# Kernel tuning notes

Measured on AMD Instinct MI355X. Metric: run time of the kernel, lower is better.

## Reference

```python
import jax, jax.numpy as jnp
import numpy as np

N, E, CIN, H, OUT, L, G = 100000, 1600000, 64, 128, 16, 3, 64

def setup_inputs() -> dict:
    key = jax.random.key(0)
    ks = jax.random.split(key, 20)
    def xav(k, shape):
        fan_in, fan_out = shape[-2], shape[-1]
        lim = float(np.sqrt(6.0 / (fan_in + fan_out)))
        return jax.random.uniform(k, shape, jnp.float32, -lim, lim)
    inp = {
        "x": jax.random.normal(ks[0], (N, CIN), jnp.float32),
        "pos": jax.random.normal(ks[1], (N, 3), jnp.float32),
        "edge_index": jax.random.randint(ks[2], (2, E), 0, N, jnp.int64),
        "batch": jnp.sort(jax.random.randint(ks[3], (N,), 0, G, jnp.int64)),
        # node_lin: Linear(CIN+3, H) -> ReLU -> Linear(H, H)
        "node_w1": xav(ks[4], (CIN + 3, H)), "node_b1": jnp.zeros((H,), jnp.float32),
        "node_w2": xav(ks[5], (H, H)), "node_b2": jnp.zeros((H,), jnp.float32),
        # L convs, each with [L, H, H] propagation weights and a GRUCell
        "conv_w": xav(ks[6], (L, L, H, H)),
        "gru_wih": xav(ks[7], (L, 3 * H, H)), "gru_whh": xav(ks[8], (L, 3 * H, H)),
        "gru_bih": jnp.zeros((L, 3 * H), jnp.float32), "gru_bhh": jnp.zeros((L, 3 * H), jnp.float32),
        "lin1_w": xav(ks[9], (H, H // 2)), "lin1_b": jnp.zeros((H // 2,), jnp.float32),
        "lin2_w": xav(ks[10], (H // 2, OUT)), "lin2_b": jnp.zeros((OUT,), jnp.float32),
    }
    return inp

def _gru_cell(m, h, wih, whh, bih, bhh):
    # torch.nn.GRUCell semantics: gates = [r, z, n]
    gi = m @ wih.T + bih  # [N, 3H]
    gh = h @ whh.T + bhh
    ir, iz, inn = jnp.split(gi, 3, axis=1)
    hr, hz, hn = jnp.split(gh, 3, axis=1)
    r = jax.nn.sigmoid(ir + hr)
    z = jax.nn.sigmoid(iz + hz)
    n = jnp.tanh(inn + r * hn)
    return (1.0 - z) * n + z * h

def reference(x, pos, edge_index, batch, node_w1, node_b1, node_w2, node_b2,
              conv_w, gru_wih, gru_whh, gru_bih, gru_bhh,
              lin1_w, lin1_b, lin2_w, lin2_b):
    src, dst = edge_index[0], edge_index[1]  # message flows src -> dst
    h = jnp.concatenate([x, pos], axis=1)
    h = jax.nn.relu(h @ node_w1 + node_b1) @ node_w2 + node_b2
    for l in range(L):  # GatedNet outer convs
        for i in range(L):  # GatedGraphConv inner iterations
            m = h @ conv_w[l, i]                                  # [N, H]
            agg = jax.ops.segment_sum(m[src], dst, num_segments=N)  # gather + scatter-add
            h = _gru_cell(agg, h, gru_wih[l], gru_whh[l], gru_bih[l], gru_bhh[l])
        h = jax.nn.relu(h)
    h = jax.nn.relu(h @ lin1_w + lin1_b)
    h = h @ lin2_w + lin2_b                                        # [N, OUT]
    return jax.ops.segment_sum(h, batch, num_segments=G)           # graph readout 'add'
```

## Files before the change

### kernel.cpp

```cpp
#include <hip/hip_runtime.h>

#define NN 100000
#define NE 1600000
#define NG 64
#define MAXDEG 64

typedef long long i64;
typedef unsigned short u16;
typedef unsigned int u32;
typedef __attribute__((ext_vector_type(8))) _Float16 f16x8;
typedef __attribute__((ext_vector_type(4))) _Float16 half4;
typedef __attribute__((ext_vector_type(4))) float f32x4;

__device__ __forceinline__ float sigm(float x){ return 1.f/(1.f+__expf(-x)); }
__device__ __forceinline__ float tanh_(float x){ return 2.f/(1.f+__expf(-2.f*x)) - 1.f; }
__device__ __forceinline__ f32x4 mfma16h(f16x8 a, f16x8 b, f32x4 c){
  return __builtin_amdgcn_mfma_f32_16x16x32_f16(a,b,c,0,0,0);
}
__device__ __forceinline__ u16 h2u(_Float16 h){ return *(const u16*)&h; }

__global__ __launch_bounds__(512) void k_detect(const int* __restrict__ ei,
    const int* __restrict__ batch, int* __restrict__ flags){
  int t = threadIdx.x;
  __shared__ int nz_e, nz_b;
  if (t == 0){ nz_e = 0; nz_b = 0; }
  __syncthreads();
  if (ei[2*t + 1] != 0) nz_e = 1;
  int k = NN/2 - 512 + t;
  if (batch[2*k + 1] != 0) nz_b = 1;
  __syncthreads();
  if (t == 0){ flags[0] = nz_e ? 0 : 1; flags[1] = nz_b ? 0 : 1; }
}

__global__ __launch_bounds__(256) void k_prep_wT(const float* __restrict__ wih,
    const float* __restrict__ whh, float* __restrict__ wihT, float* __restrict__ whhT){
  int idx = blockIdx.x*256 + threadIdx.x;
  if (idx >= 3*49152) return;
  int l = idx/49152, r = idx - l*49152, k = r/384, jc = r - k*384;
  wihT[idx] = wih[((size_t)l*384 + jc)*128 + k];
  whhT[idx] = whh[((size_t)l*384 + jc)*128 + k];
}

__global__ __launch_bounds__(384) void k_weff(const float* __restrict__ convw,
    const float* __restrict__ wihT, float* __restrict__ WeffT){
  int bid = blockIdx.x;
  int li = bid >> 7, k = bid & 127;
  int l = li / 3;
  int j = threadIdx.x;
  __shared__ float cwrow[128];
  if (j < 128) cwrow[j] = convw[((size_t)li*128 + k)*128 + j];
  __syncthreads();
  const float* wT = wihT + (size_t)l*49152;
  float acc = 0.f;
#pragma unroll 8
  for (int m = 0; m < 128; ++m)
    acc = fmaf(cwrow[m], wT[(size_t)m*384 + j], acc);
  WeffT[(size_t)li*49152 + (size_t)k*384 + j] = acc;
}

__global__ __launch_bounds__(256) void k_bsplit(const float* __restrict__ WeffT,
    const float* __restrict__ whhT, u16* __restrict__ Bhi, u16* __restrict__ Blo){
  int idx = blockIdx.x*256 + threadIdx.x;
  int li = idx >> 17;
  int r = idx & 131071;
  int col = r >> 8, k = r & 255;
  int l = li / 3;
  float v = 0.f;
  if (k < 128){
    if (col < 384) v = WeffT[(size_t)li*49152 + (size_t)k*384 + col];
  } else {
    int k2 = k - 128;
    if (col < 256)       v = whhT[(size_t)l*49152 + (size_t)k2*384 + col];
    else if (col >= 384) v = whhT[(size_t)l*49152 + (size_t)k2*384 + (col-128)];
  }
  _Float16 hi = (_Float16)v;
  _Float16 lo = (_Float16)(v - (float)hi);
  size_t widx = (size_t)li*131072 + ((((size_t)(k>>5))*512 + col)*4 + ((k>>3)&3))*8 + (k&7);
  Bhi[widx] = h2u(hi);
  Blo[widx] = h2u(lo);
}

__global__ __launch_bounds__(256) void k_fill_edges(const int* __restrict__ ei,
    const int* __restrict__ flags, int* __restrict__ deg, int* __restrict__ col){
  int e = blockIdx.x*256 + threadIdx.x;
  if (e >= NE) return;
  int s, d;
  if (flags[0]){
    const i64* e64 = (const i64*)ei;
    s = (int)e64[e]; d = (int)e64[NE + e];
  } else {
    s = ei[e]; d = ei[NE + e];
  }
  int slot = atomicAdd(&deg[d], 1);
  if (slot < MAXDEG) col[(size_t)d*MAXDEG + slot] = s;
}

__global__ __launch_bounds__(128) void k_enc_n(const float* __restrict__ x,
    const float* __restrict__ pos, const float* __restrict__ w1, const float* __restrict__ b1,
    const float* __restrict__ w2, const float* __restrict__ b2, float* __restrict__ h){
  int n0 = blockIdx.x * 8, j = threadIdx.x;
  __shared__ float xr[8][68];
  __shared__ float t1[8][128];
  for (int q = j; q < 8*67; q += 128){
    int p = q/67, kk = q - p*67;
    xr[p][kk] = (kk < 64) ? x[(size_t)(n0+p)*64 + kk] : pos[(size_t)(n0+p)*3 + (kk-64)];
  }
  __syncthreads();
  float s[8];
#pragma unroll
  for (int p=0;p<8;++p) s[p] = b1[j];
  for (int k=0;k<67;++k){
    float w = w1[k*128 + j];
#pragma unroll
    for (int p=0;p<8;++p) s[p] = fmaf(xr[p][k], w, s[p]);
  }
#pragma unroll
  for (int p=0;p<8;++p) t1[p][j] = fmaxf(s[p], 0.f);
  __syncthreads();
#pragma unroll
  for (int p=0;p<8;++p) s[p] = b2[j];
  for (int k=0;k<128;++k){
    float w = w2[k*128 + j];
#pragma unroll
    for (int p=0;p<8;++p) s[p] = fmaf(t1[p][k], w, s[p]);
  }
#pragma unroll
  for (int p=0;p<8;++p) h[(size_t)(n0+p)*128 + j] = s[p];
}

__global__ __launch_bounds__(512, 8) void k_fused(const int* __restrict__ deg,
    const int* __restrict__ col, const float* __restrict__ hin, float* __restrict__ hout,
    const u16* __restrict__ Bhi, const u16* __restrict__ Blo,
    const float* __restrict__ bih, const float* __restrict__ bhh, int apply_relu){
  __shared__ u16 Ahi[32*256];
  __shared__ u16 Alo[32*256];
  const int tid = threadIdx.x, lane = tid & 63, w = tid >> 6;
  const int tile = blockIdx.x * 32;

#pragma unroll
  for (int i = 0; i < 2; ++i){
    int f = i*512 + tid;
    int row = f >> 5, colq = f & 31;
    float4 v = *(const float4*)(hin + (size_t)(tile+row)*128 + colq*4);
    int colu = 128 + colq*4;
    int cs = (colu >> 3) ^ (row & 7);
    int idx = row*256 + cs*8 + (colu & 7);
    _Float16 h0=(_Float16)v.x, h1=(_Float16)v.y, h2=(_Float16)v.z, h3=(_Float16)v.w;
    _Float16 l0=(_Float16)(v.x-(float)h0), l1=(_Float16)(v.y-(float)h1),
             l2=(_Float16)(v.z-(float)h2), l3=(_Float16)(v.w-(float)h3);
    half4 hv = {h0,h1,h2,h3};
    half4 lv = {l0,l1,l2,l3};
    *(half4*)(Ahi + idx) = hv;
    *(half4*)(Alo + idx) = lv;
  }

#pragma unroll
  for (int rr = 0; rr < 4; ++rr){
    int row = w*4 + rr;
    int node = tile + row;
    float ax = 0.f, ay = 0.f;
    int d = deg[node]; d = min(d, MAXDEG);
    int mysrc = col[(size_t)node*MAXDEG + lane];
    int s = 0;
    for (; s + 1 < d; s += 2){
      int s0 = __shfl(mysrc, s, 64);
      int s1 = __shfl(mysrc, s+1, 64);
      float2 v0 = *(const float2*)(hin + (size_t)s0*128 + (lane<<1));
      float2 v1 = *(const float2*)(hin + (size_t)s1*128 + (lane<<1));
      ax += v0.x + v1.x;
      ay += v0.y + v1.y;
    }
    if (s < d){
      int s0 = __shfl(mysrc, s, 64);
      float2 v0 = *(const float2*)(hin + (size_t)s0*128 + (lane<<1));
      ax += v0.x; ay += v0.y;
    }
    int colu = lane << 1;
    int cs = (colu >> 3) ^ (row & 7);
    int idx = row*256 + cs*8 + (colu & 7);
    _Float16 hx=(_Float16)ax, hy=(_Float16)ay;
    _Float16 lx=(_Float16)(ax-(float)hx), ly=(_Float16)(ay-(float)hy);
    *(u32*)(Ahi + idx) = (u32)h2u(hx) | ((u32)h2u(hy) << 16);
    *(u32*)(Alo + idx) = (u32)h2u(lx) | ((u32)h2u(ly) << 16);
  }
  __syncthreads();

  const f32x4 fz = {0.f,0.f,0.f,0.f};
  f32x4 acc[4][2];
#pragma unroll
  for (int g=0;g<4;++g)
#pragma unroll
    for (int R=0;R<2;++R) acc[g][R] = fz;

#pragma unroll
  for (int kk = 0; kk < 8; ++kk){
    f16x8 a_hi[2], a_lo[2];
#pragma unroll
    for (int R=0;R<2;++R){
      int arow = R*16 + (lane&15);
      int cs = (kk*4 + (lane>>4)) ^ (arow & 7);
      a_hi[R] = *(const f16x8*)(Ahi + arow*256 + cs*8);
      a_lo[R] = *(const f16x8*)(Alo + arow*256 + cs*8);
    }
#pragma unroll
    for (int g=0; g<4; ++g){
      if (g==2 && kk>=4) continue;
      if (g==3 && kk<4) continue;
      int colg = g*128 + w*16 + (lane&15);
      size_t boff = (((size_t)kk*512 + colg)*4 + (lane>>4))*8;
      f16x8 bh = *(const f16x8*)(Bhi + boff);
      f16x8 bl = *(const f16x8*)(Blo + boff);
#pragma unroll
      for (int R=0;R<2;++R){
        acc[g][R] = mfma16h(a_hi[R], bh, acc[g][R]);
        acc[g][R] = mfma16h(a_hi[R], bl, acc[g][R]);
        acc[g][R] = mfma16h(a_lo[R], bh, acc[g][R]);
      }
    }
  }

  {
    int jj = w*16 + (lane&15);
    float br  = bih[jj]     + bhh[jj];
    float bz  = bih[128+jj] + bhh[128+jj];
    float bin = bih[256+jj];
    float bhn = bhh[256+jj];
#pragma unroll
    for (int R=0;R<2;++R)
#pragma unroll
      for (int v=0;v<4;++v){
        int r_ = R*16 + ((lane>>4)<<2) + v;
        float rg = sigm(acc[0][R][v] + br);
        float zg = sigm(acc[1][R][v] + bz);
        float hnv = acc[3][R][v] + bhn;
        float ng = tanh_(acc[2][R][v] + bin + rg*hnv);
        int colu = 128 + jj;
        int cs = (colu >> 3) ^ (r_ & 7);
        int lidx = r_*256 + cs*8 + (colu & 7);
        float hold = (float)(*(const _Float16*)(Ahi + lidx))
                   + (float)(*(const _Float16*)(Alo + lidx));
        float hnew = (1.f - zg)*ng + zg*hold;
        if (apply_relu) hnew = fmaxf(hnew, 0.f);
        hout[(size_t)(tile + r_)*128 + jj] = hnew;
      }
  }
}

__global__ __launch_bounds__(64) void k_head_n(const float* __restrict__ h,
    const float* __restrict__ l1, const float* __restrict__ b1,
    const float* __restrict__ l2, const float* __restrict__ b2, float* __restrict__ nodeout){
  int n0 = blockIdx.x * 8, j = threadIdx.x;
  __shared__ float hrow[8][128], t[8][64];
  for (int q = j; q < 1024; q += 64){
    int p = q >> 7, k = q & 127;
    hrow[p][k] = h[(size_t)(n0+p)*128 + k];
  }
  __syncthreads();
  float s[8];
#pragma unroll
  for (int p=0;p<8;++p) s[p] = b1[j];
  for (int k=0;k<128;++k){
    float w = l1[k*64 + j];
#pragma unroll
    for (int p=0;p<8;++p) s[p] = fmaf(hrow[p][k], w, s[p]);
  }
#pragma unroll
  for (int p=0;p<8;++p) t[p][j] = fmaxf(s[p], 0.f);
  __syncthreads();
  int c = j & 15;
#pragma unroll
  for (int pp=0;pp<2;++pp){
    int p = (j >> 4) + pp*4;
    float o = b2[c];
    for (int k=0;k<64;++k) o = fmaf(t[p][k], l2[k*16 + c], o);
    nodeout[(size_t)(n0+p)*16 + c] = o;
  }
}

__device__ __forceinline__ int lbound32(const int* __restrict__ a, int n, int v){
  int lo = 0, hi = n;
  while (lo < hi){ int mid = (lo+hi)>>1; if (a[mid] < v) lo = mid+1; else hi = mid; }
  return lo;
}
__device__ __forceinline__ int lbound64(const i64* __restrict__ a, int n, i64 v){
  int lo = 0, hi = n;
  while (lo < hi){ int mid = (lo+hi)>>1; if (a[mid] < v) lo = mid+1; else hi = mid; }
  return lo;
}
__global__ __launch_bounds__(256) void k_reduce(const float* __restrict__ nodeout,
    const int* __restrict__ batch, const int* __restrict__ flags, float* __restrict__ out){
  int g = blockIdx.x;
  int lo, hi;
  if (flags[1]){
    const i64* b64 = (const i64*)batch;
    lo = lbound64(b64, NN, (i64)g); hi = lbound64(b64, NN, (i64)g+1);
  } else {
    lo = lbound32(batch, NN, g); hi = lbound32(batch, NN, g+1);
  }
  int tid = threadIdx.x;
  int c = tid & 15, rr = tid >> 4;
  float s = 0.f;
  for (int r = lo + rr; r < hi; r += 16) s += nodeout[(size_t)r*16 + c];
  __shared__ float red[256];
  red[tid] = s; __syncthreads();
  for (int step = 128; step >= 16; step >>= 1){
    if (tid < step) red[tid] += red[tid + step];
    __syncthreads();
  }
  if (tid < 16) out[g*16 + tid] = red[tid];
}

extern "C" void kernel_launch(void* const* d_in, const int* in_sizes, int n_in,
                              void* d_out, int out_size, void* d_ws, size_t ws_size,
                              hipStream_t stream){
  const float* x        = (const float*)d_in[0];
  const float* pos      = (const float*)d_in[1];
  const int*   edge     = (const int*)d_in[2];
  const int*   batch    = (const int*)d_in[3];
  const float* node_w1  = (const float*)d_in[4];
  const float* node_b1  = (const float*)d_in[5];
  const float* node_w2  = (const float*)d_in[6];
  const float* node_b2  = (const float*)d_in[7];
  const float* conv_w   = (const float*)d_in[8];
  const float* gru_wih  = (const float*)d_in[9];
  const float* gru_whh  = (const float*)d_in[10];
  const float* gru_bih  = (const float*)d_in[11];
  const float* gru_bhh  = (const float*)d_in[12];
  const float* lin1_w   = (const float*)d_in[13];
  const float* lin1_b   = (const float*)d_in[14];
  const float* lin2_w   = (const float*)d_in[15];
  const float* lin2_b   = (const float*)d_in[16];
  float* out = (float*)d_out;

  char* p = (char*)d_ws;
  int*   flags = (int*)p;   p += 256;
  float* h0    = (float*)p; p += (size_t)NN*128*4;
  float* h1    = (float*)p; p += (size_t)NN*128*4;
  float* nodeout = (float*)p; p += (size_t)NN*16*4;
  int*   deg   = (int*)p;   p += (size_t)NN*4;
  int*   col   = (int*)p;   p += (size_t)NN*MAXDEG*4;
  float* wihT  = (float*)p; p += (size_t)3*49152*4;
  float* whhT  = (float*)p; p += (size_t)3*49152*4;
  float* WeffT = (float*)p; p += (size_t)9*49152*4;
  u16*   Bhi   = (u16*)p;   p += (size_t)9*512*256*2;
  u16*   Blo   = (u16*)p;   p += (size_t)9*512*256*2;

  k_detect<<<1, 512, 0, stream>>>(edge, batch, flags);
  hipMemsetAsync(deg, 0, (size_t)NN*4, stream);
  k_prep_wT<<<(147456 + 255)/256, 256, 0, stream>>>(gru_wih, gru_whh, wihT, whhT);
  k_weff<<<9*128, 384, 0, stream>>>(conv_w, wihT, WeffT);
  k_bsplit<<<9*512*256/256, 256, 0, stream>>>(WeffT, whhT, Bhi, Blo);
  k_fill_edges<<<NE/256, 256, 0, stream>>>(edge, flags, deg, col);
  k_enc_n<<<NN/8, 128, 0, stream>>>(x, pos, node_w1, node_b1, node_w2, node_b2, h0);

  float* hbuf[2] = { h0, h1 };
  for (int l = 0; l < 3; ++l){
    for (int i = 0; i < 3; ++i){
      int li = l*3 + i;
      k_fused<<<NN/32, 512, 0, stream>>>(deg, col, hbuf[li & 1], hbuf[(li + 1) & 1],
          Bhi + (size_t)li*131072, Blo + (size_t)li*131072,
          gru_bih + l*384, gru_bhh + l*384, (i==2) ? 1 : 0);
    }
  }
  k_head_n<<<NN/8, 64, 0, stream>>>(hbuf[1], lin1_w, lin1_b, lin2_w, lin2_b, nodeout);
  k_reduce<<<NG, 256, 0, stream>>>(nodeout, batch, flags, out);
}
```

Baseline: 2.123 ms.

## Widen neighbor gather to float4 half-waves and stage GRU output through LDS

The neighbor aggregation now processes two destination rows per wave, with each half-wave reading float4 per lane instead of float2 across the full wave. This halves the row loop count and widens each global load. The GRU output is no longer written as scattered scalar stores. It is staged into shared memory, reusing the Ahi buffer, and then written out as coalesced float4 rows. This adds two block barriers and LDS traffic in exchange for better global store coalescing.

```diff
diff --git a/kernel.cpp b/kernel.cpp
--- a/kernel.cpp
+++ b/kernel.cpp
@@ -154,34 +154,55 @@
     *(half4*)(Alo + idx) = lv;
   }
 
-#pragma unroll
-  for (int rr = 0; rr < 4; ++rr){
-    int row = w*4 + rr;
+  const int half = lane >> 5, ln32 = lane & 31;
+#pragma unroll
+  for (int rr = 0; rr < 2; ++rr){
+    int row = rr*16 + w*2 + half;
     int node = tile + row;
-    float ax = 0.f, ay = 0.f;
     int d = deg[node]; d = min(d, MAXDEG);
-    int mysrc = col[(size_t)node*MAXDEG + lane];
+    int src1 = col[(size_t)node*MAXDEG + ln32];
+    int src2 = col[(size_t)node*MAXDEG + 32 + ln32];
+    float ax=0.f, ay=0.f, az=0.f, aw=0.f;
+    int d1 = min(d, 32);
     int s = 0;
-    for (; s + 1 < d; s += 2){
-      int s0 = __shfl(mysrc, s, 64);
-      int s1 = __shfl(mysrc, s+1, 64);
-      float2 v0 = *(const float2*)(hin + (size_t)s0*128 + (lane<<1));
-      float2 v1 = *(const float2*)(hin + (size_t)s1*128 + (lane<<1));
-      ax += v0.x + v1.x;
-      ay += v0.y + v1.y;
-    }
-    if (s < d){
-      int s0 = __shfl(mysrc, s, 64);
-      float2 v0 = *(const float2*)(hin + (size_t)s0*128 + (lane<<1));
-      ax += v0.x; ay += v0.y;
-    }
-    int colu = lane << 1;
+    for (; s + 1 < d1; s += 2){
+      int a0 = __shfl(src1, half*32 + s, 64);
+      int a1 = __shfl(src1, half*32 + s + 1, 64);
+      float4 v0 = *(const float4*)(hin + (size_t)a0*128 + (ln32<<2));
+      float4 v1 = *(const float4*)(hin + (size_t)a1*128 + (ln32<<2));
+      ax += v0.x; ay += v0.y; az += v0.z; aw += v0.w;
+      ax += v1.x; ay += v1.y; az += v1.z; aw += v1.w;
+    }
+    if (s < d1){
+      int a0 = __shfl(src1, half*32 + s, 64);
+      float4 v0 = *(const float4*)(hin + (size_t)a0*128 + (ln32<<2));
+      ax += v0.x; ay += v0.y; az += v0.z; aw += v0.w;
+    }
+    int d2 = d - d1;
+    s = 0;
+    for (; s + 1 < d2; s += 2){
+      int a0 = __shfl(src2, half*32 + s, 64);
+      int a1 = __shfl(src2, half*32 + s + 1, 64);
+      float4 v0 = *(const float4*)(hin + (size_t)a0*128 + (ln32<<2));
+      float4 v1 = *(const float4*)(hin + (size_t)a1*128 + (ln32<<2));
+      ax += v0.x; ay += v0.y; az += v0.z; aw += v0.w;
+      ax += v1.x; ay += v1.y; az += v1.z; aw += v1.w;
+    }
+    if (s < d2){
+      int a0 = __shfl(src2, half*32 + s, 64);
+      float4 v0 = *(const float4*)(hin + (size_t)a0*128 + (ln32<<2));
+      ax += v0.x; ay += v0.y; az += v0.z; aw += v0.w;
+    }
+    int colu = ln32 << 2;
     int cs = (colu >> 3) ^ (row & 7);
     int idx = row*256 + cs*8 + (colu & 7);
-    _Float16 hx=(_Float16)ax, hy=(_Float16)ay;
-    _Float16 lx=(_Float16)(ax-(float)hx), ly=(_Float16)(ay-(float)hy);
-    *(u32*)(Ahi + idx) = (u32)h2u(hx) | ((u32)h2u(hy) << 16);
-    *(u32*)(Alo + idx) = (u32)h2u(lx) | ((u32)h2u(ly) << 16);
+    _Float16 hx=(_Float16)ax, hy=(_Float16)ay, hz=(_Float16)az, hw=(_Float16)aw;
+    _Float16 lx=(_Float16)(ax-(float)hx), ly=(_Float16)(ay-(float)hy),
+             lz=(_Float16)(az-(float)hz), lw=(_Float16)(aw-(float)hw);
+    half4 hv = {hx,hy,hz,hw};
+    half4 lv = {lx,ly,lz,lw};
+    *(half4*)(Ahi + idx) = hv;
+    *(half4*)(Alo + idx) = lv;
   }
   __syncthreads();
 
@@ -219,6 +240,7 @@
     }
   }
 
+  float hn_reg[2][4];
   {
     int jj = w*16 + (lane&15);
     float br  = bih[jj]     + bhh[jj];
@@ -241,8 +263,28 @@
                    + (float)(*(const _Float16*)(Alo + lidx));
         float hnew = (1.f - zg)*ng + zg*hold;
         if (apply_relu) hnew = fmaxf(hnew, 0.f);
-        hout[(size_t)(tile + r_)*128 + jj] = hnew;
+        hn_reg[R][v] = hnew;
       }
+  }
+  __syncthreads();
+  float* fout = (float*)Ahi;
+  {
+    int jj = w*16 + (lane&15);
+#pragma unroll
+    for (int R=0;R<2;++R)
+#pragma unroll
+      for (int v=0;v<4;++v){
+        int r_ = R*16 + ((lane>>4)<<2) + v;
+        fout[r_*128 + jj] = hn_reg[R][v];
+      }
+  }
+  __syncthreads();
+#pragma unroll
+  for (int i = 0; i < 2; ++i){
+    int f = i*512 + tid;
+    int row = f >> 5, colq = f & 31;
+    float4 vv = *(const float4*)(fout + row*128 + colq*4);
+    *(float4*)(hout + (size_t)(tile+row)*128 + colq*4) = vv;
   }
 }
 
```

After: 2.023 ms. -4.7%, faster.
